# Kernel tuning notes

Hardware: AMD Instinct MI355X
Metric: run time of the kernel (lower is better)

## Reference

```python
import jax, jax.numpy as jnp
import numpy as np

XYZ_MIN, XYZ_MAX = -1.0, 1.0
GRID = 160                                   # world_size per axis
VOXEL_SIZE = (XYZ_MAX - XYZ_MIN) / GRID      # 0.0125
ALPHA_INIT = 0.01
ACT_SHIFT = float(np.log(1.0 / (1.0 - ALPHA_INIT) - 1.0))
NEAR, FAR = 0.2, 6.0
STEPSIZE = 0.5
INTERVAL = STEPSIZE * 1.0                    # voxel_size_ratio == 1
N_SAMPLES = int(np.linalg.norm(np.array([GRID + 1] * 3)) / STEPSIZE) + 1  # 558
BG = 1.0


def trilinear_sample(grid, xyz):
    """grid: [C,X,Y,Z]; xyz: [...,3] world coords. F.grid_sample bilinear, align_corners=True."""
    size = np.array(grid.shape[1:])
    u = (xyz - XYZ_MIN) / (XYZ_MAX - XYZ_MIN)          # [...,3] in [0,1] (inside bbox)
    idx = u * (size - 1).astype(np.float32)            # align_corners=True index space
    i0 = jnp.floor(idx).astype(jnp.int32)
    frac = idx - i0
    lo = jnp.clip(i0, 0, size - 1)
    hi = jnp.clip(i0 + 1, 0, size - 1)
    out = 0.0
    for bx in (0, 1):
        for by in (0, 1):
            for bz in (0, 1):
                ix = hi[..., 0] if bx else lo[..., 0]
                iy = hi[..., 1] if by else lo[..., 1]
                iz = hi[..., 2] if bz else lo[..., 2]
                w = ((frac[..., 0] if bx else 1.0 - frac[..., 0]) *
                     (frac[..., 1] if by else 1.0 - frac[..., 1]) *
                     (frac[..., 2] if bz else 1.0 - frac[..., 2]))
                out = out + grid[:, ix, iy, iz] * w[None]
    return jnp.moveaxis(out, 0, -1)                    # [...,C]


def setup_inputs() -> dict:
    key = jax.random.key(0)
    k1, k2, k3, k4 = jax.random.split(key, 4)
    N = 16384
    o = jax.random.normal(k1, (N, 3), dtype=jnp.float32)
    rays_o = o / jnp.linalg.norm(o, axis=-1, keepdims=True) * 3.0   # on sphere r=3, outside bbox
    d = -rays_o + 0.3 * jax.random.normal(k2, (N, 3), dtype=jnp.float32)
    rays_d = d / jnp.linalg.norm(d, axis=-1, keepdims=True)         # point toward origin
    density = jax.random.normal(k3, (1, 1, GRID, GRID, GRID), dtype=jnp.float32)
    k0 = 0.5 * jax.random.normal(k4, (1, 3, GRID, GRID, GRID), dtype=jnp.float32)
    return {"rays_o": rays_o, "rays_d": rays_d, "density": density, "k0": k0}


def reference(rays_o, rays_d, density, k0):
    # --- sample_ray (is_train=False) ---
    vec = jnp.where(rays_d == 0, jnp.float32(1e-6), rays_d)
    rate_a = (XYZ_MAX - rays_o) / vec
    rate_b = (XYZ_MIN - rays_o) / vec
    t_min = jnp.clip(jnp.minimum(rate_a, rate_b).max(-1), NEAR, FAR)   # [N]
    t_max = jnp.clip(jnp.maximum(rate_a, rate_b).min(-1), NEAR, FAR)
    ray_oob = t_max < t_min                                            # ray misses bbox
    rng = jnp.arange(N_SAMPLES, dtype=rays_o.dtype)                    # [S]
    step = STEPSIZE * VOXEL_SIZE * rng
    interpx = t_min[:, None] + step[None, :] / jnp.linalg.norm(rays_d, axis=-1, keepdims=True)  # [N,S]
    rays_pts = rays_o[:, None, :] + rays_d[:, None, :] * interpx[..., None]                     # [N,S,3]
    mask_oob = ray_oob[:, None] | ((rays_pts < XYZ_MIN) | (rays_pts > XYZ_MAX)).any(-1)         # [N,S]

    # --- density -> alpha (activate_density), zero outside bbox ---
    dens = trilinear_sample(density[0], rays_pts)[..., 0]              # [N,S]
    alpha = jnp.where(mask_oob, 0.0,
                      1.0 - jnp.exp(-jax.nn.softplus(dens + ACT_SHIFT) * INTERVAL))

    # --- alpha compositing ---
    ones = jnp.ones_like(alpha[:, :1])
    alphainv_cum = jnp.concatenate([ones, jnp.cumprod(1.0 - alpha, axis=-1)], axis=-1)  # [N,S+1]
    weights = alpha * alphainv_cum[:, :-1]                             # [N,S]

    # --- color (rgbnet is None -> sigmoid of k0) and ray marching ---
    rgb = jax.nn.sigmoid(trilinear_sample(k0[0], rays_pts))            # [N,S,3]
    rgb_marched = jnp.einsum('ns,nsc->nc', weights, rgb) + alphainv_cum[:, -1:] * BG
    return rgb_marched
```

## Files before the change

kernel.cpp:

```cpp
#include <hip/hip_runtime.h>
#include <math.h>

#define G 160
#define GM1 159
#define NS 558
#define CHSTRIDE (160 * 160 * 160)
#define G3 (160 * 160 * 160)

#define DENS_SCALE (10.0f / 255.0f)
#define DENS_BIAS  (-5.0f)
#define COL_SCALE  (7.0f / 255.0f)
#define COL_BIAS   (-3.5f)

#define NBUCKET 512
#define MAXRAYS 16384


__device__ __forceinline__ unsigned int q8(float v, float bias, float invscale) {
    return (unsigned int)lrintf(fminf(fmaxf((v - bias) * invscale, 0.f), 255.f));
}

__global__ __launch_bounds__(1024) void prep_fused(
    const float* __restrict__ dens,
    const float* __restrict__ k0,
    const float* __restrict__ rays_o,
    const float* __restrict__ rays_d,
    unsigned int* __restrict__ packed,
    unsigned int* __restrict__ order, int N)
{
    __shared__ unsigned short skeys[MAXRAYS];
    __shared__ unsigned int hist[NBUCKET];
    __shared__ unsigned int tmp[NBUCKET];
    __shared__ unsigned int offs[NBUCKET];

    const int tid = threadIdx.x;

    if (blockIdx.x == 0) {
        for (int i = tid; i < NBUCKET; i += 1024) hist[i] = 0;
        __syncthreads();
        for (int r = tid; r < N; r += 1024) {
            const float ox = rays_o[r * 3 + 0], oy = rays_o[r * 3 + 1], oz = rays_o[r * 3 + 2];
            const float dx = rays_d[r * 3 + 0], dy = rays_d[r * 3 + 1], dz = rays_d[r * 3 + 2];
            const float vx = (dx == 0.f) ? 1e-6f : dx;
            const float vy = (dy == 0.f) ? 1e-6f : dy;
            const float vz = (dz == 0.f) ? 1e-6f : dz;
            const float rax = (1.f - ox) / vx, rbx = (-1.f - ox) / vx;
            const float ray_ = (1.f - oy) / vy, rby = (-1.f - oy) / vy;
            const float raz = (1.f - oz) / vz, rbz = (-1.f - oz) / vz;
            float tmin = fmaxf(fmaxf(fminf(rax, rbx), fminf(ray_, rby)), fminf(raz, rbz));
            tmin = fminf(fmaxf(tmin, 0.2f), 6.0f);
            const float px = fminf(fmaxf(fmaf(dx, tmin, ox), -1.f), 1.f);
            const float py = fminf(fmaxf(fmaf(dy, tmin, oy), -1.f), 1.f);
            const float pz = fminf(fmaxf(fmaf(dz, tmin, oz), -1.f), 1.f);
            const int cx = min(7, (int)((px + 1.f) * 4.f));
            const int cy = min(7, (int)((py + 1.f) * 4.f));
            const int cz = min(7, (int)((pz + 1.f) * 4.f));
            const unsigned int key = (unsigned int)((cx << 6) | (cy << 3) | cz);
            skeys[r] = (unsigned short)key;
            atomicAdd(&hist[key], 1u);
        }
        __syncthreads();
        if (tid < NBUCKET) tmp[tid] = hist[tid];
        __syncthreads();
        for (int off = 1; off < NBUCKET; off <<= 1) {
            unsigned int v = 0;
            if (tid < NBUCKET && tid >= off) v = tmp[tid - off];
            __syncthreads();
            if (tid < NBUCKET) tmp[tid] += v;
            __syncthreads();
        }
        if (tid < NBUCKET) offs[tid] = tmp[tid] - hist[tid];
        __syncthreads();
        for (int r = tid; r < N; r += 1024) {
            const unsigned int pos = atomicAdd(&offs[skeys[r]], 1u);
            order[pos] = (unsigned int)r;
        }
    } else {
        const int base = ((blockIdx.x - 1) * 1024 + tid) * 4;
        if (base + 3 < G3) {
            const float4 d = *(const float4*)(dens + base);
            const float4 r = *(const float4*)(k0 + base);
            const float4 g = *(const float4*)(k0 + CHSTRIDE + base);
            const float4 b = *(const float4*)(k0 + 2 * CHSTRIDE + base);
            const float dis = 255.f / 10.f, cis = 255.f / 7.f;
            uint4 o;
            o.x = q8(d.x, DENS_BIAS, dis) | (q8(r.x, COL_BIAS, cis) << 8) |
                  (q8(g.x, COL_BIAS, cis) << 16) | (q8(b.x, COL_BIAS, cis) << 24);
            o.y = q8(d.y, DENS_BIAS, dis) | (q8(r.y, COL_BIAS, cis) << 8) |
                  (q8(g.y, COL_BIAS, cis) << 16) | (q8(b.y, COL_BIAS, cis) << 24);
            o.z = q8(d.z, DENS_BIAS, dis) | (q8(r.z, COL_BIAS, cis) << 8) |
                  (q8(g.z, COL_BIAS, cis) << 16) | (q8(b.z, COL_BIAS, cis) << 24);
            o.w = q8(d.w, DENS_BIAS, dis) | (q8(r.w, COL_BIAS, cis) << 8) |
                  (q8(g.w, COL_BIAS, cis) << 16) | (q8(b.w, COL_BIAS, cis) << 24);
            *(uint4*)(packed + base) = o;
        }
    }
}


__device__ __forceinline__ float ub(unsigned int q, int c) {
    return (float)((q >> (c * 8)) & 0xffu);
}

struct SampleData {
    unsigned int q000, q001, q010, q011, q100, q101, q110, q111;
    float w000, w001, w010, w011, w100, w101, w110, w111;
    float amask;
};

__device__ __forceinline__ SampleData fetch_sample(
    const unsigned int* __restrict__ pg,
    float ex, float ey, float ez, float gx, float gy, float gz, int s)
{
    SampleData r;
    const float sF = (float)s;
    const float fx = fmaf(gx, sF, ex);
    const float fy = fmaf(gy, sF, ey);
    const float fz = fmaf(gz, sF, ez);
    const float mn  = fminf(fminf(fx, fy), fz);
    const float mx_ = fmaxf(fmaxf(fx, fy), fz);
    r.amask = (mn >= 0.f && mx_ <= 159.f) ? 1.f : 0.f;
    const float cfx = __builtin_amdgcn_fmed3f(fx, 0.f, 159.f);
    const float cfy = __builtin_amdgcn_fmed3f(fy, 0.f, 159.f);
    const float cfz = __builtin_amdgcn_fmed3f(fz, 0.f, 159.f);
    const int x0 = (int)cfx; const float tx = cfx - (float)x0;
    const int y0 = (int)cfy; const float ty = cfy - (float)y0;
    const int z0 = (int)cfz; const float tz = cfz - (float)z0;
    const int x1 = min(x0 + 1, GM1);
    const int y1 = min(y0 + 1, GM1);
    const float mx = 1.f - tx, my = 1.f - ty, mz = 1.f - tz;
    const float w00 = mx * my, w01 = mx * ty, w10 = tx * my, w11 = tx * ty;
    r.w000 = w00 * mz; r.w001 = w00 * tz;
    r.w010 = w01 * mz; r.w011 = w01 * tz;
    r.w100 = w10 * mz; r.w101 = w10 * tz;
    r.w110 = w11 * mz; r.w111 = w11 * tz;
    const int xg0 = x0 * G, xg1 = x1 * G;
    const int i00 = (xg0 + y0) * G + z0;
    const int i01 = (xg0 + y1) * G + z0;
    const int i10 = (xg1 + y0) * G + z0;
    const int i11 = (xg1 + y1) * G + z0;
    r.q000 = pg[i00]; r.q001 = pg[i00 + 1];
    r.q010 = pg[i01]; r.q011 = pg[i01 + 1];
    r.q100 = pg[i10]; r.q101 = pg[i10 + 1];
    r.q110 = pg[i11]; r.q111 = pg[i11 + 1];
    return r;
}

__device__ __forceinline__ void composite(const SampleData& d, int lane,
    float& T, float& ar, float& ag, float& ab)
{
    const float ACT_SHIFT = -4.59511985013459f;
    float acc[4];
    #pragma unroll
    for (int ch = 0; ch < 4; ++ch) {
        acc[ch] = d.w000 * ub(d.q000, ch) + d.w001 * ub(d.q001, ch) +
                  d.w010 * ub(d.q010, ch) + d.w011 * ub(d.q011, ch) +
                  d.w100 * ub(d.q100, ch) + d.w101 * ub(d.q101, ch) +
                  d.w110 * ub(d.q110, ch) + d.w111 * ub(d.q111, ch);
    }
    const float dens = fmaf(acc[0], DENS_SCALE, DENS_BIAS);
    const float vr   = fmaf(acc[1], COL_SCALE,  COL_BIAS);
    const float vg   = fmaf(acc[2], COL_SCALE,  COL_BIAS);
    const float vb   = fmaf(acc[3], COL_SCALE,  COL_BIAS);
    const float e = __expf(dens + ACT_SHIFT);
    const float oma = __builtin_amdgcn_rsqf(1.f + e);
    const float alpha = (1.f - oma) * d.amask;
    const float cr = __builtin_amdgcn_rcpf(1.f + __expf(-vr));
    const float cg = __builtin_amdgcn_rcpf(1.f + __expf(-vg));
    const float cb = __builtin_amdgcn_rcpf(1.f + __expf(-vb));

    const float one_m_a = 1.f - alpha;
    float incl = one_m_a;
    #pragma unroll
    for (int off = 1; off < 64; off <<= 1) {
        const float v = __shfl_up(incl, off, 64);
        if (lane >= off) incl *= v;
    }
    const float excl = incl * __builtin_amdgcn_rcpf(one_m_a);
    const float w = alpha * T * excl;
    ar = fmaf(w, cr, ar);
    ag = fmaf(w, cg, ag);
    ab = fmaf(w, cb, ab);
    T *= __shfl(incl, 63, 64);
}

__global__ __launch_bounds__(256) void dvgo_render_u8(
    const float* __restrict__ rays_o,
    const float* __restrict__ rays_d,
    const unsigned int* __restrict__ pg,
    const unsigned int* __restrict__ order,
    float* __restrict__ out, int N)
{
    unsigned int bid = blockIdx.x;
    const unsigned int nblk = gridDim.x;
    if ((nblk & 511u) == 0u) {
        const unsigned int xcd  = bid & 7u;
        const unsigned int step = bid >> 3;
        const unsigned int cseq = step >> 6;
        const unsigned int pos  = step & 63u;
        bid = (cseq * 8u + xcd) * 64u + pos;
    } else if ((nblk & 7u) == 0u) {
        bid = (bid & 7u) * (nblk >> 3) + (bid >> 3);
    }
    const int slot = (int)(bid * 4 + (threadIdx.x >> 6));
    const int lane = (int)(threadIdx.x & 63u);
    if (slot >= N) return;
    const int wave = order ? (int)order[slot] : slot;

    const float ox = rays_o[wave * 3 + 0], oy = rays_o[wave * 3 + 1], oz = rays_o[wave * 3 + 2];
    const float dx = rays_d[wave * 3 + 0], dy = rays_d[wave * 3 + 1], dz = rays_d[wave * 3 + 2];
    const float inv_norm = __builtin_amdgcn_rsqf(dx * dx + dy * dy + dz * dz);

    const float vx = (dx == 0.f) ? 1e-6f : dx;
    const float vy = (dy == 0.f) ? 1e-6f : dy;
    const float vz = (dz == 0.f) ? 1e-6f : dz;
    const float rax = (1.f - ox) / vx, rbx = (-1.f - ox) / vx;
    const float ray_ = (1.f - oy) / vy, rby = (-1.f - oy) / vy;
    const float raz = (1.f - oz) / vz, rbz = (-1.f - oz) / vz;
    float tmin = fmaxf(fmaxf(fminf(rax, rbx), fminf(ray_, rby)), fminf(raz, rbz));
    float tmax = fminf(fminf(fmaxf(rax, rbx), fmaxf(ray_, rby)), fmaxf(raz, rbz));
    tmin = fminf(fmaxf(tmin, 0.2f), 6.0f);
    tmax = fminf(fmaxf(tmax, 0.2f), 6.0f);

    const float dt = 0.00625f * inv_norm;

    const float ex = (fmaf(dx, tmin, ox) + 1.f) * 79.5f;
    const float ey = (fmaf(dy, tmin, oy) + 1.f) * 79.5f;
    const float ez = (fmaf(dz, tmin, oz) + 1.f) * 79.5f;
    const float gx = dx * dt * 79.5f;
    const float gy = dy * dt * 79.5f;
    const float gz = dz * dt * 79.5f;

    int n_samp = 0;
    if (!(tmax < tmin)) n_samp = min(NS, (int)((tmax - tmin) / dt) + 2);
    const int n_chunks = (n_samp + 63) >> 6;

    float T = 1.f;
    float ar = 0.f, ag = 0.f, ab = 0.f;

    if (n_chunks > 0) {
        SampleData sd0 = fetch_sample(pg, ex, ey, ez, gx, gy, gz, lane);
        SampleData sd1;
        if (n_chunks > 1) sd1 = fetch_sample(pg, ex, ey, ez, gx, gy, gz, 64 + lane);
        for (int c = 0; c < n_chunks; ++c) {
            SampleData sd2;
            if (c + 2 < n_chunks)
                sd2 = fetch_sample(pg, ex, ey, ez, gx, gy, gz, ((c + 2) << 6) + lane);

            composite(sd0, lane, T, ar, ag, ab);

            sd0 = sd1;
            sd1 = sd2;
        }
    }

    #pragma unroll
    for (int off = 32; off > 0; off >>= 1) {
        ar += __shfl_down(ar, off, 64);
        ag += __shfl_down(ag, off, 64);
        ab += __shfl_down(ab, off, 64);
    }
    if (lane == 0) {
        out[wave * 3 + 0] = ar + T;
        out[wave * 3 + 1] = ag + T;
        out[wave * 3 + 2] = ab + T;
    }
}


__global__ __launch_bounds__(256) void dvgo_render_f32(
    const float* __restrict__ rays_o,
    const float* __restrict__ rays_d,
    const float* __restrict__ dens_g,
    const float* __restrict__ k0_g,
    float* __restrict__ out, int N)
{
    const int wave = (int)((blockIdx.x * 256u + threadIdx.x) >> 6);
    const int lane = (int)(threadIdx.x & 63u);
    if (wave >= N) return;

    const float ox = rays_o[wave * 3 + 0], oy = rays_o[wave * 3 + 1], oz = rays_o[wave * 3 + 2];
    const float dx = rays_d[wave * 3 + 0], dy = rays_d[wave * 3 + 1], dz = rays_d[wave * 3 + 2];
    const float inv_norm = rsqrtf(dx * dx + dy * dy + dz * dz);

    const float vx = (dx == 0.f) ? 1e-6f : dx;
    const float vy = (dy == 0.f) ? 1e-6f : dy;
    const float vz = (dz == 0.f) ? 1e-6f : dz;
    const float rax = (1.f - ox) / vx, rbx = (-1.f - ox) / vx;
    const float ray_ = (1.f - oy) / vy, rby = (-1.f - oy) / vy;
    const float raz = (1.f - oz) / vz, rbz = (-1.f - oz) / vz;
    float tmin = fmaxf(fmaxf(fminf(rax, rbx), fminf(ray_, rby)), fminf(raz, rbz));
    float tmax = fminf(fminf(fmaxf(rax, rbx), fmaxf(ray_, rby)), fmaxf(raz, rbz));
    tmin = fminf(fmaxf(tmin, 0.2f), 6.0f);
    tmax = fminf(fmaxf(tmax, 0.2f), 6.0f);
    const bool ray_oob = (tmax < tmin);

    const float dt = 0.00625f * inv_norm;
    const float ACT_SHIFT = -4.59511985013459f;

    float T = 1.f;
    float ar = 0.f, ag = 0.f, ab = 0.f;

    for (int s0 = 0; s0 < NS; s0 += 64) {
        const int s = s0 + lane;
        float alpha = 0.f, cr = 0.f, cg = 0.f, cb = 0.f;
        bool valid = false;
        if (!ray_oob && s < NS) {
            const float t = tmin + dt * (float)s;
            const float px = fmaf(dx, t, ox);
            const float py = fmaf(dy, t, oy);
            const float pz = fmaf(dz, t, oz);
            if (px >= -1.f && px <= 1.f && py >= -1.f && py <= 1.f &&
                pz >= -1.f && pz <= 1.f) {
                valid = true;
                const float fx = (px + 1.f) * 79.5f;
                const float fy = (py + 1.f) * 79.5f;
                const float fz = (pz + 1.f) * 79.5f;
                int x0 = (int)fx; const float tx = fx - (float)x0;
                int y0 = (int)fy; const float ty = fy - (float)y0;
                int z0 = (int)fz; const float tz = fz - (float)z0;
                x0 = min(x0, GM1); y0 = min(y0, GM1); z0 = min(z0, GM1);
                const int x1 = min(x0 + 1, GM1);
                const int y1 = min(y0 + 1, GM1);
                const int z1 = min(z0 + 1, GM1);

                const float mx = 1.f - tx, my = 1.f - ty, mz = 1.f - tz;
                const float w00 = mx * my, w01 = mx * ty, w10 = tx * my, w11 = tx * ty;
                const float w000 = w00 * mz, w001 = w00 * tz;
                const float w010 = w01 * mz, w011 = w01 * tz;
                const float w100 = w10 * mz, w101 = w10 * tz;
                const float w110 = w11 * mz, w111 = w11 * tz;

                const int b00 = (x0 * G + y0) * G;
                const int b01 = (x0 * G + y1) * G;
                const int b10 = (x1 * G + y0) * G;
                const int b11 = (x1 * G + y1) * G;

                const float dens =
                    w000 * dens_g[b00 + z0] + w001 * dens_g[b00 + z1] +
                    w010 * dens_g[b01 + z0] + w011 * dens_g[b01 + z1] +
                    w100 * dens_g[b10 + z0] + w101 * dens_g[b10 + z1] +
                    w110 * dens_g[b11 + z0] + w111 * dens_g[b11 + z1];

                const float e = __expf(dens + ACT_SHIFT);
                alpha = 1.f - rsqrtf(1.f + e);

                #pragma unroll
                for (int ch = 0; ch < 3; ++ch) {
                    const float* k0c = k0_g + ch * CHSTRIDE;
                    const float v =
                        w000 * k0c[b00 + z0] + w001 * k0c[b00 + z1] +
                        w010 * k0c[b01 + z0] + w011 * k0c[b01 + z1] +
                        w100 * k0c[b10 + z0] + w101 * k0c[b10 + z1] +
                        w110 * k0c[b11 + z0] + w111 * k0c[b11 + z1];
                    const float sg = 1.f / (1.f + __expf(-v));
                    if (ch == 0) cr = sg; else if (ch == 1) cg = sg; else cb = sg;
                }
            }
        }

        float incl = 1.f - alpha;
        #pragma unroll
        for (int off = 1; off < 64; off <<= 1) {
            const float v = __shfl_up(incl, off, 64);
            if (lane >= off) incl *= v;
        }
        float excl = __shfl_up(incl, 1, 64);
        if (lane == 0) excl = 1.f;

        const float w = alpha * T * excl;
        ar = fmaf(w, cr, ar);
        ag = fmaf(w, cg, ag);
        ab = fmaf(w, cb, ab);

        T *= __shfl(incl, 63, 64);

        if (__ballot(valid) == 0ull) break;
        if (T < 1e-5f) break;
    }

    #pragma unroll
    for (int off = 32; off > 0; off >>= 1) {
        ar += __shfl_down(ar, off, 64);
        ag += __shfl_down(ag, off, 64);
        ab += __shfl_down(ab, off, 64);
    }
    if (lane == 0) {
        out[wave * 3 + 0] = ar + T;
        out[wave * 3 + 1] = ag + T;
        out[wave * 3 + 2] = ab + T;
    }
}

extern "C" void kernel_launch(void* const* d_in, const int* in_sizes, int n_in,
                              void* d_out, int out_size, void* d_ws, size_t ws_size,
                              hipStream_t stream) {
    const float* rays_o  = (const float*)d_in[0];
    const float* rays_d  = (const float*)d_in[1];
    const float* density = (const float*)d_in[2];
    const float* k0      = (const float*)d_in[3];
    float* out = (float*)d_out;
    const int N = in_sizes[0] / 3;

    const int blocks = (N * 64 + 255) / 256;

    const size_t grid_b  = (size_t)G3 * 4;
    const size_t need = grid_b + (size_t)N * 4;

    if (ws_size >= need && N <= MAXRAYS) {
        unsigned int* packed = (unsigned int*)d_ws;
        unsigned int* order  = (unsigned int*)((char*)d_ws + grid_b);
        const int pack_blocks = (G3 + 4095) / 4096;
        prep_fused<<<pack_blocks + 1, 1024, 0, stream>>>(density, k0, rays_o, rays_d,
                                                         packed, order, N);
        dvgo_render_u8<<<blocks, 256, 0, stream>>>(rays_o, rays_d, packed, order, out, N);
    } else {
        dvgo_render_f32<<<blocks, 256, 0, stream>>>(rays_o, rays_d, density, k0, out, N);
    }
}
```

Before: 88.09 us.

## Split volume into x-halves mapped to XCD groups, composite partials per half

Each ray is rendered twice, once per x-half of the grid. Blocks are mapped so that XCDs 0-3 handle the low half and XCDs 4-7 the high half, with rays sorted per half by entry cell. A combine kernel then merges the two partial transmittance/color results in front-to-back order. The intent is to cut each XCD's working set of the packed grid to about half, so it stays in the per-XCD L2 cache. The cost is twice as many waves, extra per-ray setup, an extra sort pass and a third kernel launch, and the default path now requires N == MAXRAYS.

```diff
diff --git a/kernel.cpp b/kernel.cpp
--- a/kernel.cpp
+++ b/kernel.cpp
@@ -12,7 +12,7 @@
 #define COL_SCALE  (7.0f / 255.0f)
 #define COL_BIAS   (-3.5f)
 
-#define NBUCKET 512
+#define NCELL 512
 #define MAXRAYS 16384
 
 
@@ -29,51 +29,56 @@
     unsigned int* __restrict__ order, int N)
 {
     __shared__ unsigned short skeys[MAXRAYS];
-    __shared__ unsigned int hist[NBUCKET];
-    __shared__ unsigned int tmp[NBUCKET];
-    __shared__ unsigned int offs[NBUCKET];
+    __shared__ unsigned int hist[NCELL];
+    __shared__ unsigned int tmp[NCELL];
+    __shared__ unsigned int offs[NCELL];
 
     const int tid = threadIdx.x;
 
     if (blockIdx.x == 0) {
-        for (int i = tid; i < NBUCKET; i += 1024) hist[i] = 0;
-        __syncthreads();
-        for (int r = tid; r < N; r += 1024) {
-            const float ox = rays_o[r * 3 + 0], oy = rays_o[r * 3 + 1], oz = rays_o[r * 3 + 2];
-            const float dx = rays_d[r * 3 + 0], dy = rays_d[r * 3 + 1], dz = rays_d[r * 3 + 2];
-            const float vx = (dx == 0.f) ? 1e-6f : dx;
-            const float vy = (dy == 0.f) ? 1e-6f : dy;
-            const float vz = (dz == 0.f) ? 1e-6f : dz;
-            const float rax = (1.f - ox) / vx, rbx = (-1.f - ox) / vx;
-            const float ray_ = (1.f - oy) / vy, rby = (-1.f - oy) / vy;
-            const float raz = (1.f - oz) / vz, rbz = (-1.f - oz) / vz;
-            float tmin = fmaxf(fmaxf(fminf(rax, rbx), fminf(ray_, rby)), fminf(raz, rbz));
-            tmin = fminf(fmaxf(tmin, 0.2f), 6.0f);
-            const float px = fminf(fmaxf(fmaf(dx, tmin, ox), -1.f), 1.f);
-            const float py = fminf(fmaxf(fmaf(dy, tmin, oy), -1.f), 1.f);
-            const float pz = fminf(fmaxf(fmaf(dz, tmin, oz), -1.f), 1.f);
-            const int cx = min(7, (int)((px + 1.f) * 4.f));
-            const int cy = min(7, (int)((py + 1.f) * 4.f));
-            const int cz = min(7, (int)((pz + 1.f) * 4.f));
-            const unsigned int key = (unsigned int)((cx << 6) | (cy << 3) | cz);
-            skeys[r] = (unsigned short)key;
-            atomicAdd(&hist[key], 1u);
-        }
-        __syncthreads();
-        if (tid < NBUCKET) tmp[tid] = hist[tid];
-        __syncthreads();
-        for (int off = 1; off < NBUCKET; off <<= 1) {
-            unsigned int v = 0;
-            if (tid < NBUCKET && tid >= off) v = tmp[tid - off];
+        for (int h = 0; h < 2; ++h) {
+            for (int i = tid; i < NCELL; i += 1024) hist[i] = 0;
             __syncthreads();
-            if (tid < NBUCKET) tmp[tid] += v;
+            const float xlo = h ? 0.f : -1.f;
+            const float xhi = h ? 1.f : 0.f;
+            for (int r = tid; r < N; r += 1024) {
+                const float ox = rays_o[r * 3 + 0], oy = rays_o[r * 3 + 1], oz = rays_o[r * 3 + 2];
+                const float dx = rays_d[r * 3 + 0], dy = rays_d[r * 3 + 1], dz = rays_d[r * 3 + 2];
+                const float vx = (dx == 0.f) ? 1e-6f : dx;
+                const float vy = (dy == 0.f) ? 1e-6f : dy;
+                const float vz = (dz == 0.f) ? 1e-6f : dz;
+                const float raxh = (xhi - ox) / vx, rbxh = (xlo - ox) / vx;
+                const float ray_ = (1.f - oy) / vy, rby = (-1.f - oy) / vy;
+                const float raz = (1.f - oz) / vz, rbz = (-1.f - oz) / vz;
+                float tminH = fmaxf(fmaxf(fminf(raxh, rbxh), fminf(ray_, rby)), fminf(raz, rbz));
+                tminH = fminf(fmaxf(tminH, 0.2f), 6.0f);
+                const float px = fminf(fmaxf(fmaf(dx, tminH, ox), -1.f), 1.f);
+                const float py = fminf(fmaxf(fmaf(dy, tminH, oy), -1.f), 1.f);
+                const float pz = fminf(fmaxf(fmaf(dz, tminH, oz), -1.f), 1.f);
+                const int cx = min(7, (int)((px + 1.f) * 4.f));
+                const int cy = min(7, (int)((py + 1.f) * 4.f));
+                const int cz = min(7, (int)((pz + 1.f) * 4.f));
+                const unsigned int key = (unsigned int)((cx << 6) | (cy << 3) | cz);
+                skeys[r] = (unsigned short)key;
+                atomicAdd(&hist[key], 1u);
+            }
             __syncthreads();
-        }
-        if (tid < NBUCKET) offs[tid] = tmp[tid] - hist[tid];
-        __syncthreads();
-        for (int r = tid; r < N; r += 1024) {
-            const unsigned int pos = atomicAdd(&offs[skeys[r]], 1u);
-            order[pos] = (unsigned int)r;
+            if (tid < NCELL) tmp[tid] = hist[tid];
+            __syncthreads();
+            for (int off = 1; off < NCELL; off <<= 1) {
+                unsigned int v = 0;
+                if (tid < NCELL && tid >= off) v = tmp[tid - off];
+                __syncthreads();
+                if (tid < NCELL) tmp[tid] += v;
+                __syncthreads();
+            }
+            if (tid < NCELL) offs[tid] = tmp[tid] - hist[tid];
+            __syncthreads();
+            for (int r = tid; r < N; r += 1024) {
+                const unsigned int pos = atomicAdd(&offs[skeys[r]], 1u);
+                order[h * N + pos] = (unsigned int)r;
+            }
+            __syncthreads();
         }
     } else {
         const int base = ((blockIdx.x - 1) * 1024 + tid) * 4;
@@ -110,7 +115,7 @@
 
 __device__ __forceinline__ SampleData fetch_sample(
     const unsigned int* __restrict__ pg,
-    float ex, float ey, float ez, float gx, float gy, float gz, int s)
+    float ex, float ey, float ez, float gx, float gy, float gz, int s, int half)
 {
     SampleData r;
     const float sF = (float)s;
@@ -119,7 +124,8 @@
     const float fz = fmaf(gz, sF, ez);
     const float mn  = fminf(fminf(fx, fy), fz);
     const float mx_ = fmaxf(fmaxf(fx, fy), fz);
-    r.amask = (mn >= 0.f && mx_ <= 159.f) ? 1.f : 0.f;
+    const bool hs = half ? (fx >= 79.5f) : (fx < 79.5f);
+    r.amask = (mn >= 0.f && mx_ <= 159.f && hs) ? 1.f : 0.f;
     const float cfx = __builtin_amdgcn_fmed3f(fx, 0.f, 159.f);
     const float cfy = __builtin_amdgcn_fmed3f(fy, 0.f, 159.f);
     const float cfz = __builtin_amdgcn_fmed3f(fz, 0.f, 159.f);
@@ -184,31 +190,27 @@
     T *= __shfl(incl, 63, 64);
 }
 
-__global__ __launch_bounds__(256) void dvgo_render_u8(
+__global__ __launch_bounds__(256) void dvgo_render_split(
     const float* __restrict__ rays_o,
     const float* __restrict__ rays_d,
     const unsigned int* __restrict__ pg,
     const unsigned int* __restrict__ order,
-    float* __restrict__ out, int N)
-{
-    unsigned int bid = blockIdx.x;
-    const unsigned int nblk = gridDim.x;
-    if ((nblk & 511u) == 0u) {
-        const unsigned int xcd  = bid & 7u;
-        const unsigned int step = bid >> 3;
-        const unsigned int cseq = step >> 6;
-        const unsigned int pos  = step & 63u;
-        bid = (cseq * 8u + xcd) * 64u + pos;
-    } else if ((nblk & 7u) == 0u) {
-        bid = (bid & 7u) * (nblk >> 3) + (bid >> 3);
-    }
-    const int slot = (int)(bid * 4 + (threadIdx.x >> 6));
+    float4* __restrict__ partials, int N)
+{
+    const unsigned int bid  = blockIdx.x;
+    const unsigned int xcd  = bid & 7u;
+    const int half          = (int)(xcd >> 2);
+    const unsigned int xcdh = xcd & 3u;
+    const unsigned int j    = bid >> 3;
+    const unsigned int cseq = j >> 6;
+    const unsigned int pos  = j & 63u;
+    const unsigned int bidp = (cseq * 4u + xcdh) * 64u + pos;
+    const int slot = (int)(bidp * 4u + (threadIdx.x >> 6));
     const int lane = (int)(threadIdx.x & 63u);
-    if (slot >= N) return;
-    const int wave = order ? (int)order[slot] : slot;
-
-    const float ox = rays_o[wave * 3 + 0], oy = rays_o[wave * 3 + 1], oz = rays_o[wave * 3 + 2];
-    const float dx = rays_d[wave * 3 + 0], dy = rays_d[wave * 3 + 1], dz = rays_d[wave * 3 + 2];
+    const int ray  = (int)order[half * N + slot];
+
+    const float ox = rays_o[ray * 3 + 0], oy = rays_o[ray * 3 + 1], oz = rays_o[ray * 3 + 2];
+    const float dx = rays_d[ray * 3 + 0], dy = rays_d[ray * 3 + 1], dz = rays_d[ray * 3 + 2];
     const float inv_norm = __builtin_amdgcn_rsqf(dx * dx + dy * dy + dz * dz);
 
     const float vx = (dx == 0.f) ? 1e-6f : dx;
@@ -217,12 +219,32 @@
     const float rax = (1.f - ox) / vx, rbx = (-1.f - ox) / vx;
     const float ray_ = (1.f - oy) / vy, rby = (-1.f - oy) / vy;
     const float raz = (1.f - oz) / vz, rbz = (-1.f - oz) / vz;
-    float tmin = fmaxf(fmaxf(fminf(rax, rbx), fminf(ray_, rby)), fminf(raz, rbz));
-    float tmax = fminf(fminf(fmaxf(rax, rbx), fmaxf(ray_, rby)), fmaxf(raz, rbz));
+    const float tyzmin = fmaxf(fminf(ray_, rby), fminf(raz, rbz));
+    const float tyzmax = fminf(fmaxf(ray_, rby), fmaxf(raz, rbz));
+    float tmin = fmaxf(tyzmin, fminf(rax, rbx));
+    float tmax = fminf(tyzmax, fmaxf(rax, rbx));
     tmin = fminf(fmaxf(tmin, 0.2f), 6.0f);
     tmax = fminf(fmaxf(tmax, 0.2f), 6.0f);
 
     const float dt = 0.00625f * inv_norm;
+
+    int n_samp = 0;
+    if (!(tmax < tmin)) n_samp = min(NS, (int)((tmax - tmin) / dt) + 2);
+
+    const float xlo = half ? 0.f : -1.f;
+    const float xhi = half ? 1.f : 0.f;
+    const float raxh = (xhi - ox) / vx, rbxh = (xlo - ox) / vx;
+    float tminH = fmaxf(tyzmin, fminf(raxh, rbxh));
+    float tmaxH = fminf(tyzmax, fmaxf(raxh, rbxh));
+    tminH = fminf(fmaxf(tminH, 0.2f), 6.0f);
+    tmaxH = fminf(fmaxf(tmaxH, 0.2f), 6.0f);
+
+    int s0 = 0, s1 = 0;
+    if (n_samp > 0 && !(tmaxH < tminH)) {
+        s0 = max(0, (int)((tminH - tmin) / dt) - 2);
+        s1 = min(n_samp, (int)((tmaxH - tmin) / dt) + 3);
+    }
+    const int n_chunks = (s1 > s0) ? ((s1 - s0 + 63) >> 6) : 0;
 
     const float ex = (fmaf(dx, tmin, ox) + 1.f) * 79.5f;
     const float ey = (fmaf(dy, tmin, oy) + 1.f) * 79.5f;
@@ -231,21 +253,17 @@
     const float gy = dy * dt * 79.5f;
     const float gz = dz * dt * 79.5f;
 
-    int n_samp = 0;
-    if (!(tmax < tmin)) n_samp = min(NS, (int)((tmax - tmin) / dt) + 2);
-    const int n_chunks = (n_samp + 63) >> 6;
-
     float T = 1.f;
     float ar = 0.f, ag = 0.f, ab = 0.f;
 
     if (n_chunks > 0) {
-        SampleData sd0 = fetch_sample(pg, ex, ey, ez, gx, gy, gz, lane);
+        SampleData sd0 = fetch_sample(pg, ex, ey, ez, gx, gy, gz, s0 + lane, half);
         SampleData sd1;
-        if (n_chunks > 1) sd1 = fetch_sample(pg, ex, ey, ez, gx, gy, gz, 64 + lane);
+        if (n_chunks > 1) sd1 = fetch_sample(pg, ex, ey, ez, gx, gy, gz, s0 + 64 + lane, half);
         for (int c = 0; c < n_chunks; ++c) {
             SampleData sd2;
             if (c + 2 < n_chunks)
-                sd2 = fetch_sample(pg, ex, ey, ez, gx, gy, gz, ((c + 2) << 6) + lane);
+                sd2 = fetch_sample(pg, ex, ey, ez, gx, gy, gz, s0 + ((c + 2) << 6) + lane, half);
 
             composite(sd0, lane, T, ar, ag, ab);
 
@@ -261,10 +279,40 @@
         ab += __shfl_down(ab, off, 64);
     }
     if (lane == 0) {
-        out[wave * 3 + 0] = ar + T;
-        out[wave * 3 + 1] = ag + T;
-        out[wave * 3 + 2] = ab + T;
-    }
+        partials[half * N + ray] = make_float4(ar, ag, ab, T);
+    }
+}
+
+
+__global__ __launch_bounds__(256) void combine_halves(
+    const float* __restrict__ rays_o,
+    const float* __restrict__ rays_d,
+    const float4* __restrict__ partials,
+    float* __restrict__ out, int N)
+{
+    const int r = blockIdx.x * 256 + threadIdx.x;
+    if (r >= N) return;
+    const float ox = rays_o[r * 3 + 0], oy = rays_o[r * 3 + 1], oz = rays_o[r * 3 + 2];
+    const float dx = rays_d[r * 3 + 0], dy = rays_d[r * 3 + 1], dz = rays_d[r * 3 + 2];
+    const float vx = (dx == 0.f) ? 1e-6f : dx;
+    const float vy = (dy == 0.f) ? 1e-6f : dy;
+    const float vz = (dz == 0.f) ? 1e-6f : dz;
+    const float rax = (1.f - ox) / vx, rbx = (-1.f - ox) / vx;
+    const float ray_ = (1.f - oy) / vy, rby = (-1.f - oy) / vy;
+    const float raz = (1.f - oz) / vz, rbz = (-1.f - oz) / vz;
+    const float tyzmin = fmaxf(fminf(ray_, rby), fminf(raz, rbz));
+    float tmin = fmaxf(tyzmin, fminf(rax, rbx));
+    tmin = fminf(fmaxf(tmin, 0.2f), 6.0f);
+    const float ex = (fmaf(dx, tmin, ox) + 1.f) * 79.5f;
+
+    const float4 a = partials[r];
+    const float4 b = partials[N + r];
+    float4 f, s;
+    if (ex < 79.5f) { f = a; s = b; } else { f = b; s = a; }
+    const float Ttot = f.w * s.w;
+    out[r * 3 + 0] = f.x + f.w * s.x + Ttot;
+    out[r * 3 + 1] = f.y + f.w * s.y + Ttot;
+    out[r * 3 + 2] = f.z + f.w * s.z + Ttot;
 }
 
 
@@ -402,19 +450,24 @@
     float* out = (float*)d_out;
     const int N = in_sizes[0] / 3;
 
-    const int blocks = (N * 64 + 255) / 256;
-
-    const size_t grid_b  = (size_t)G3 * 4;
-    const size_t need = grid_b + (size_t)N * 4;
-
-    if (ws_size >= need && N <= MAXRAYS) {
+    const size_t grid_b    = (size_t)G3 * 4;
+    const size_t order_b   = (size_t)2 * N * 4;
+    const size_t part_b    = (size_t)2 * N * 16;
+    const size_t need = grid_b + order_b + part_b;
+
+    if (ws_size >= need && N == MAXRAYS) {
         unsigned int* packed = (unsigned int*)d_ws;
         unsigned int* order  = (unsigned int*)((char*)d_ws + grid_b);
+        float4* partials     = (float4*)((char*)d_ws + grid_b + order_b);
         const int pack_blocks = (G3 + 4095) / 4096;
         prep_fused<<<pack_blocks + 1, 1024, 0, stream>>>(density, k0, rays_o, rays_d,
                                                          packed, order, N);
-        dvgo_render_u8<<<blocks, 256, 0, stream>>>(rays_o, rays_d, packed, order, out, N);
+        const int rblocks = (2 * N) / 4;
+        dvgo_render_split<<<rblocks, 256, 0, stream>>>(rays_o, rays_d, packed, order,
+                                                       partials, N);
+        combine_halves<<<(N + 255) / 256, 256, 0, stream>>>(rays_o, rays_d, partials, out, N);
     } else {
+        const int blocks = (N * 64 + 255) / 256;
         dvgo_render_f32<<<blocks, 256, 0, stream>>>(rays_o, rays_d, density, k0, out, N);
     }
 }
```

Measured after the change: 114.8 us. 30.4% more time.

## Split each ray into two segments at x=0 and bucket them per XCD half

Applied to the files above, without the earlier changes.

Each ray is split into two segments at the plane x=0. The segments are keyed by the spatial cell of their entry and exit points, with the x-half folded into the key. Segments in the x<0 and x>=0 halves go to disjoint groups of XCDs, so each XCD's L2 only needs to hold half of the packed grid. Partial colour and transmittance per segment are written to a workspace and merged by a new combine kernel. This adds a second render task per ray, a sentinel-filled order array, an extra kernel launch, and recomputation of the keys in the prep block. The fast path is now limited to N exactly equal to MAXRAYS.

```diff
diff --git a/kernel.cpp b/kernel.cpp
--- a/kernel.cpp
+++ b/kernel.cpp
@@ -12,12 +12,53 @@
 #define COL_SCALE  (7.0f / 255.0f)
 #define COL_BIAS   (-3.5f)
 
-#define NBUCKET 512
+#define NBKT 1024
 #define MAXRAYS 16384
+#define SENT 0xFFFFFFFFu
 
 
 __device__ __forceinline__ unsigned int q8(float v, float bias, float invscale) {
     return (unsigned int)lrintf(fminf(fmaxf((v - bias) * invscale, 0.f), 255.f));
+}
+
+__device__ __forceinline__ void task_keys(
+    const float* __restrict__ rays_o, const float* __restrict__ rays_d, int r,
+    unsigned int& keyA, unsigned int& keyB)
+{
+    const float ox = rays_o[r * 3 + 0], oy = rays_o[r * 3 + 1], oz = rays_o[r * 3 + 2];
+    const float dx = rays_d[r * 3 + 0], dy = rays_d[r * 3 + 1], dz = rays_d[r * 3 + 2];
+    const float vx = (dx == 0.f) ? 1e-6f : dx;
+    const float vy = (dy == 0.f) ? 1e-6f : dy;
+    const float vz = (dz == 0.f) ? 1e-6f : dz;
+    const float rax = (1.f - ox) / vx, rbx = (-1.f - ox) / vx;
+    const float ray_ = (1.f - oy) / vy, rby = (-1.f - oy) / vy;
+    const float raz = (1.f - oz) / vz, rbz = (-1.f - oz) / vz;
+    float tmin = fmaxf(fmaxf(fminf(rax, rbx), fminf(ray_, rby)), fminf(raz, rbz));
+    float tmax = fminf(fminf(fmaxf(rax, rbx), fmaxf(ray_, rby)), fmaxf(raz, rbz));
+    tmin = fminf(fmaxf(tmin, 0.2f), 6.0f);
+    tmax = fminf(fmaxf(tmax, 0.2f), 6.0f);
+    {
+        const float pxr = fmaf(dx, tmin, ox);
+        const float px = fminf(fmaxf(pxr, -1.f), 1.f);
+        const float py = fminf(fmaxf(fmaf(dy, tmin, oy), -1.f), 1.f);
+        const float pz = fminf(fmaxf(fmaf(dz, tmin, oz), -1.f), 1.f);
+        const int cx = min(7, (int)((px + 1.f) * 4.f));
+        const int cy = min(7, (int)((py + 1.f) * 4.f));
+        const int cz = min(7, (int)((pz + 1.f) * 4.f));
+        const unsigned int h = (pxr >= 0.f) ? 1u : 0u;
+        keyA = (h << 9) | (unsigned int)((cx << 6) | (cy << 3) | cz);
+    }
+    {
+        const float pxr = fmaf(dx, tmax, ox);
+        const float px = fminf(fmaxf(pxr, -1.f), 1.f);
+        const float py = fminf(fmaxf(fmaf(dy, tmax, oy), -1.f), 1.f);
+        const float pz = fminf(fmaxf(fmaf(dz, tmax, oz), -1.f), 1.f);
+        const int cx = min(7, (int)((px + 1.f) * 4.f));
+        const int cy = min(7, (int)((py + 1.f) * 4.f));
+        const int cz = min(7, (int)((pz + 1.f) * 4.f));
+        const unsigned int h = (pxr >= 0.f) ? 1u : 0u;
+        keyB = (h << 9) | (unsigned int)((cx << 6) | (cy << 3) | cz);
+    }
 }
 
 __global__ __launch_bounds__(1024) void prep_fused(
@@ -28,52 +69,42 @@
     unsigned int* __restrict__ packed,
     unsigned int* __restrict__ order, int N)
 {
-    __shared__ unsigned short skeys[MAXRAYS];
-    __shared__ unsigned int hist[NBUCKET];
-    __shared__ unsigned int tmp[NBUCKET];
-    __shared__ unsigned int offs[NBUCKET];
+    __shared__ unsigned int hist[NBKT];
+    __shared__ unsigned int tmp[NBKT];
 
     const int tid = threadIdx.x;
 
     if (blockIdx.x == 0) {
-        for (int i = tid; i < NBUCKET; i += 1024) hist[i] = 0;
+        for (int i = tid; i < NBKT; i += 1024) hist[i] = 0;
         __syncthreads();
         for (int r = tid; r < N; r += 1024) {
-            const float ox = rays_o[r * 3 + 0], oy = rays_o[r * 3 + 1], oz = rays_o[r * 3 + 2];
-            const float dx = rays_d[r * 3 + 0], dy = rays_d[r * 3 + 1], dz = rays_d[r * 3 + 2];
-            const float vx = (dx == 0.f) ? 1e-6f : dx;
-            const float vy = (dy == 0.f) ? 1e-6f : dy;
-            const float vz = (dz == 0.f) ? 1e-6f : dz;
-            const float rax = (1.f - ox) / vx, rbx = (-1.f - ox) / vx;
-            const float ray_ = (1.f - oy) / vy, rby = (-1.f - oy) / vy;
-            const float raz = (1.f - oz) / vz, rbz = (-1.f - oz) / vz;
-            float tmin = fmaxf(fmaxf(fminf(rax, rbx), fminf(ray_, rby)), fminf(raz, rbz));
-            tmin = fminf(fmaxf(tmin, 0.2f), 6.0f);
-            const float px = fminf(fmaxf(fmaf(dx, tmin, ox), -1.f), 1.f);
-            const float py = fminf(fmaxf(fmaf(dy, tmin, oy), -1.f), 1.f);
-            const float pz = fminf(fmaxf(fmaf(dz, tmin, oz), -1.f), 1.f);
-            const int cx = min(7, (int)((px + 1.f) * 4.f));
-            const int cy = min(7, (int)((py + 1.f) * 4.f));
-            const int cz = min(7, (int)((pz + 1.f) * 4.f));
-            const unsigned int key = (unsigned int)((cx << 6) | (cy << 3) | cz);
-            skeys[r] = (unsigned short)key;
-            atomicAdd(&hist[key], 1u);
+            unsigned int ka, kb;
+            task_keys(rays_o, rays_d, r, ka, kb);
+            atomicAdd(&hist[ka], 1u);
+            atomicAdd(&hist[kb], 1u);
         }
         __syncthreads();
-        if (tid < NBUCKET) tmp[tid] = hist[tid];
+        tmp[tid] = hist[tid];
         __syncthreads();
-        for (int off = 1; off < NBUCKET; off <<= 1) {
-            unsigned int v = 0;
-            if (tid < NBUCKET && tid >= off) v = tmp[tid - off];
+        for (int off = 1; off < NBKT; off <<= 1) {
+            const unsigned int v = (tid >= off) ? tmp[tid - off] : 0u;
             __syncthreads();
-            if (tid < NBUCKET) tmp[tid] += v;
+            tmp[tid] += v;
             __syncthreads();
         }
-        if (tid < NBUCKET) offs[tid] = tmp[tid] - hist[tid];
+        const unsigned int cnt0 = tmp[511];
+        unsigned int off0 = tmp[tid] - hist[tid];
+        if (tid >= 512) off0 += (2u * (unsigned int)N - cnt0);
+        hist[tid] = off0;
+        for (int i = tid; i < 4 * N; i += 1024) order[i] = SENT;
         __syncthreads();
         for (int r = tid; r < N; r += 1024) {
-            const unsigned int pos = atomicAdd(&offs[skeys[r]], 1u);
-            order[pos] = (unsigned int)r;
+            unsigned int ka, kb;
+            task_keys(rays_o, rays_d, r, ka, kb);
+            const unsigned int pa = atomicAdd(&hist[ka], 1u);
+            order[pa] = ((unsigned int)r << 1) | 0u;
+            const unsigned int pb = atomicAdd(&hist[kb], 1u);
+            order[pb] = ((unsigned int)r << 1) | 1u;
         }
     } else {
         const int base = ((blockIdx.x - 1) * 1024 + tid) * 4;
@@ -184,31 +215,30 @@
     T *= __shfl(incl, 63, 64);
 }
 
-__global__ __launch_bounds__(256) void dvgo_render_u8(
+__global__ __launch_bounds__(256) void dvgo_render_seg(
     const float* __restrict__ rays_o,
     const float* __restrict__ rays_d,
     const unsigned int* __restrict__ pg,
     const unsigned int* __restrict__ order,
-    float* __restrict__ out, int N)
-{
-    unsigned int bid = blockIdx.x;
-    const unsigned int nblk = gridDim.x;
-    if ((nblk & 511u) == 0u) {
-        const unsigned int xcd  = bid & 7u;
-        const unsigned int step = bid >> 3;
-        const unsigned int cseq = step >> 6;
-        const unsigned int pos  = step & 63u;
-        bid = (cseq * 8u + xcd) * 64u + pos;
-    } else if ((nblk & 7u) == 0u) {
-        bid = (bid & 7u) * (nblk >> 3) + (bid >> 3);
-    }
-    const int slot = (int)(bid * 4 + (threadIdx.x >> 6));
+    float4* __restrict__ partials, int N)
+{
+    const unsigned int bid  = blockIdx.x;
+    const unsigned int xcd  = bid & 7u;
+    const int half          = (int)(xcd >> 2);
+    const unsigned int xcdh = xcd & 3u;
+    const unsigned int j    = bid >> 3;
+    const unsigned int cseq = j >> 6;
+    const unsigned int pos  = j & 63u;
+    const unsigned int bidp = (cseq * 4u + xcdh) * 64u + pos;
+    const int slot = (int)(bidp * 4u + (threadIdx.x >> 6));
     const int lane = (int)(threadIdx.x & 63u);
-    if (slot >= N) return;
-    const int wave = order ? (int)order[slot] : slot;
-
-    const float ox = rays_o[wave * 3 + 0], oy = rays_o[wave * 3 + 1], oz = rays_o[wave * 3 + 2];
-    const float dx = rays_d[wave * 3 + 0], dy = rays_d[wave * 3 + 1], dz = rays_d[wave * 3 + 2];
+    const unsigned int task = order[half * 2 * N + slot];
+    if (task == SENT) return;
+    const int ray = (int)(task >> 1);
+    const int seg = (int)(task & 1u);
+
+    const float ox = rays_o[ray * 3 + 0], oy = rays_o[ray * 3 + 1], oz = rays_o[ray * 3 + 2];
+    const float dx = rays_d[ray * 3 + 0], dy = rays_d[ray * 3 + 1], dz = rays_d[ray * 3 + 2];
     const float inv_norm = __builtin_amdgcn_rsqf(dx * dx + dy * dy + dz * dz);
 
     const float vx = (dx == 0.f) ? 1e-6f : dx;
@@ -224,6 +254,19 @@
 
     const float dt = 0.00625f * inv_norm;
 
+    int n_samp = 0;
+    if (!(tmax < tmin)) n_samp = min(NS, (int)((tmax - tmin) / dt) + 2);
+    const int nch = (n_samp + 63) >> 6;
+
+    const float t_cross = (0.f - ox) / vx;
+    const float sc = (t_cross - tmin) / dt;
+    int kc = (int)floorf(sc * (1.f / 64.f) + 0.5f);
+    kc = max(0, min(kc, nch));
+
+    const int cb = seg ? kc : 0;
+    const int ce = seg ? nch : kc;
+    const int ncl = ce - cb;
+
     const float ex = (fmaf(dx, tmin, ox) + 1.f) * 79.5f;
     const float ey = (fmaf(dy, tmin, oy) + 1.f) * 79.5f;
     const float ez = (fmaf(dz, tmin, oz) + 1.f) * 79.5f;
@@ -231,21 +274,17 @@
     const float gy = dy * dt * 79.5f;
     const float gz = dz * dt * 79.5f;
 
-    int n_samp = 0;
-    if (!(tmax < tmin)) n_samp = min(NS, (int)((tmax - tmin) / dt) + 2);
-    const int n_chunks = (n_samp + 63) >> 6;
-
     float T = 1.f;
     float ar = 0.f, ag = 0.f, ab = 0.f;
 
-    if (n_chunks > 0) {
-        SampleData sd0 = fetch_sample(pg, ex, ey, ez, gx, gy, gz, lane);
+    if (ncl > 0) {
+        SampleData sd0 = fetch_sample(pg, ex, ey, ez, gx, gy, gz, (cb << 6) + lane);
         SampleData sd1;
-        if (n_chunks > 1) sd1 = fetch_sample(pg, ex, ey, ez, gx, gy, gz, 64 + lane);
-        for (int c = 0; c < n_chunks; ++c) {
+        if (ncl > 1) sd1 = fetch_sample(pg, ex, ey, ez, gx, gy, gz, ((cb + 1) << 6) + lane);
+        for (int c = 0; c < ncl; ++c) {
             SampleData sd2;
-            if (c + 2 < n_chunks)
-                sd2 = fetch_sample(pg, ex, ey, ez, gx, gy, gz, ((c + 2) << 6) + lane);
+            if (c + 2 < ncl)
+                sd2 = fetch_sample(pg, ex, ey, ez, gx, gy, gz, ((cb + c + 2) << 6) + lane);
 
             composite(sd0, lane, T, ar, ag, ab);
 
@@ -261,10 +300,22 @@
         ab += __shfl_down(ab, off, 64);
     }
     if (lane == 0) {
-        out[wave * 3 + 0] = ar + T;
-        out[wave * 3 + 1] = ag + T;
-        out[wave * 3 + 2] = ab + T;
-    }
+        partials[seg * N + ray] = make_float4(ar, ag, ab, T);
+    }
+}
+
+
+__global__ __launch_bounds__(256) void combine_segs(
+    const float4* __restrict__ partials,
+    float* __restrict__ out, int N)
+{
+    const int r = blockIdx.x * 256 + threadIdx.x;
+    if (r >= N) return;
+    const float4 a = partials[r];
+    const float4 b = partials[N + r];
+    out[r * 3 + 0] = a.x + a.w * b.x + a.w * b.w;
+    out[r * 3 + 1] = a.y + a.w * b.y + a.w * b.w;
+    out[r * 3 + 2] = a.z + a.w * b.z + a.w * b.w;
 }
 
 
@@ -402,19 +453,24 @@
     float* out = (float*)d_out;
     const int N = in_sizes[0] / 3;
 
-    const int blocks = (N * 64 + 255) / 256;
-
     const size_t grid_b  = (size_t)G3 * 4;
-    const size_t need = grid_b + (size_t)N * 4;
-
-    if (ws_size >= need && N <= MAXRAYS) {
+    const size_t order_b = (size_t)4 * N * 4;
+    const size_t part_b  = (size_t)2 * N * 16;
+    const size_t need = grid_b + order_b + part_b;
+
+    if (ws_size >= need && N == MAXRAYS) {
         unsigned int* packed = (unsigned int*)d_ws;
         unsigned int* order  = (unsigned int*)((char*)d_ws + grid_b);
+        float4* partials     = (float4*)((char*)d_ws + grid_b + order_b);
         const int pack_blocks = (G3 + 4095) / 4096;
         prep_fused<<<pack_blocks + 1, 1024, 0, stream>>>(density, k0, rays_o, rays_d,
                                                          packed, order, N);
-        dvgo_render_u8<<<blocks, 256, 0, stream>>>(rays_o, rays_d, packed, order, out, N);
+        const int rblocks = (4 * N) / 4;
+        dvgo_render_seg<<<rblocks, 256, 0, stream>>>(rays_o, rays_d, packed, order,
+                                                     partials, N);
+        combine_segs<<<(N + 255) / 256, 256, 0, stream>>>(partials, out, N);
     } else {
+        const int blocks = (N * 64 + 255) / 256;
         dvgo_render_f32<<<blocks, 256, 0, stream>>>(rays_o, rays_d, density, k0, out, N);
     }
 }
```

Result: slower. 111.6 us (+26.6%).
